# Optimization experiments

Measured on AMD Instinct MI355X. Metric: run time of the kernel, lower is better.

Reference implementation:

```python
import jax, jax.numpy as jnp
import numpy as np

B, L, DM, DI, N, K, NL, DTR, VOCAB, P = 8, 256, 1024, 2048, 16, 4, 4, 128, 99, 97


def setup_inputs() -> dict:
    key = jax.random.key(0)
    ks = jax.random.split(key, 12)
    tokens = jax.random.randint(ks[0], (B, L), 0, VOCAB)
    tok_emb = 0.02 * jax.random.normal(ks[1], (VOCAB, DM), dtype=jnp.float32)
    pos_emb = 0.02 * jax.random.normal(ks[2], (L, DM), dtype=jnp.float32)
    ln_w = jnp.ones((NL, DM), jnp.float32)
    ln_b = jnp.zeros((NL, DM), jnp.float32)
    in_proj_w = jax.random.normal(ks[3], (NL, 2 * DI, DM), dtype=jnp.float32) / np.sqrt(DM)
    conv_w = jax.random.normal(ks[4], (NL, DI, K), dtype=jnp.float32) / np.sqrt(K)
    conv_b = jnp.zeros((NL, DI), jnp.float32)
    xproj_w = jax.random.normal(ks[5], (NL, DTR + 2 * N, DI), dtype=jnp.float32) / np.sqrt(DI)
    s = DTR ** -0.5
    dt_w = jax.random.uniform(ks[6], (NL, DI, DTR), minval=-s, maxval=s, dtype=jnp.float32)
    dt = jnp.exp(jax.random.uniform(ks[7], (NL, DI), dtype=jnp.float32) * (np.log(0.1) - np.log(0.001)) + np.log(0.001))
    dt = jnp.clip(dt, 1e-4)
    dt_b = dt + jnp.log(-jnp.expm1(-dt))
    A_log = jnp.broadcast_to(jnp.log(jnp.arange(1, N + 1, dtype=jnp.float32)), (NL, DI, N)) + jnp.zeros((NL, DI, N))
    D_param = jnp.ones((NL, DI), jnp.float32)
    out_proj_w = jax.random.normal(ks[8], (NL, DM, DI), dtype=jnp.float32) / np.sqrt(DI)
    fnorm_w = jnp.ones((DM,), jnp.float32)
    fnorm_b = jnp.zeros((DM,), jnp.float32)
    head_w = jax.random.normal(ks[9], (P, DM), dtype=jnp.float32) / np.sqrt(DM)
    return dict(tokens=tokens, tok_emb=tok_emb, pos_emb=pos_emb, ln_w=ln_w, ln_b=ln_b,
                in_proj_w=in_proj_w, conv_w=conv_w, conv_b=conv_b, xproj_w=xproj_w,
                dt_w=dt_w, dt_b=dt_b, A_log=A_log, D_param=D_param,
                out_proj_w=out_proj_w, fnorm_w=fnorm_w, fnorm_b=fnorm_b, head_w=head_w)


def layernorm(x, w, b):
    m = x.mean(-1, keepdims=True)
    v = ((x - m) ** 2).mean(-1, keepdims=True)
    return (x - m) * jax.lax.rsqrt(v + 1e-5) * w + b


def causal_dw_conv(x, w, b):
    # x: (B,L,DI), w: (DI,K) depthwise, torch Conv1d(padding=K-1)[..., :L] == causal
    Lx = x.shape[1]
    xp = jnp.pad(x, ((0, 0), (K - 1, 0), (0, 0)))
    y = sum(w[:, k] * xp[:, k:k + Lx, :] for k in range(K))
    return y + b


def selective_ssm(x, xpw, dtw, dtb, Alog, Dp):
    # x: (B,L,DI)
    xp = x @ xpw.T                                # (B,L,DTR+2N)
    dt_r = xp[..., :DTR]
    Bm = xp[..., DTR:DTR + N]                     # (B,L,N)
    Cm = xp[..., DTR + N:]                        # (B,L,N)
    delta = jax.nn.softplus(dt_r @ dtw.T + dtb)   # (B,L,DI)
    A = -jnp.exp(Alog)                            # (DI,N)
    dA = jnp.exp(delta[..., None] * A)            # (B,L,DI,N)
    dBx = delta[..., None] * Bm[:, :, None, :] * x[..., None]  # (B,L,DI,N)

    def step(h, inp):
        dA_t, dBx_t, C_t = inp
        h = dA_t * h + dBx_t
        return h, jnp.einsum('bdn,bn->bd', h, C_t)

    h0 = jnp.zeros((x.shape[0], DI, N), x.dtype)
    _, ys = jax.lax.scan(step, h0, (jnp.moveaxis(dA, 1, 0), jnp.moveaxis(dBx, 1, 0), jnp.moveaxis(Cm, 1, 0)))
    y = jnp.moveaxis(ys, 0, 1)                    # (B,L,DI)
    return y + x * Dp


def mamba_block(h, lnw, lnb, ipw, cw, cb, xpw, dtw, dtb, Alog, Dp, opw):
    residual = h
    x = layernorm(h, lnw, lnb)
    xz = x @ ipw.T                                # (B,L,2*DI)
    x_branch, z_gate = xz[..., :DI], xz[..., DI:]
    x_branch = jax.nn.silu(causal_dw_conv(x_branch, cw, cb))
    y = selective_ssm(x_branch, xpw, dtw, dtb, Alog, Dp)
    y = y * jax.nn.silu(z_gate)
    return y @ opw.T + residual


def reference(tokens, tok_emb, pos_emb, ln_w, ln_b, in_proj_w, conv_w, conv_b, xproj_w,
              dt_w, dt_b, A_log, D_param, out_proj_w, fnorm_w, fnorm_b, head_w):
    h = tok_emb[tokens] + pos_emb[None, :tokens.shape[1]]
    for i in range(NL):
        h = mamba_block(h, ln_w[i], ln_b[i], in_proj_w[i], conv_w[i], conv_b[i],
                        xproj_w[i], dt_w[i], dt_b[i], A_log[i], D_param[i], out_proj_w[i])
    h = layernorm(h, fnorm_w, fnorm_b)
    return h[:, -1, :] @ head_w.T                 # (B,P)
```

## Files before the change

### kernel.cpp

```cpp
#include <hip/hip_runtime.h>
#include <hip/hip_bf16.h>
#include <cstdint>
#include <cstddef>

#define B_    8
#define L_    256
#define DM_   1024
#define DI_   2048
#define N_    16
#define K_    4
#define NL_   4
#define DTR_  128
#define P_    97
#define XPD_  160
#define CHUNK_ 32
#define NC_   8

typedef __attribute__((ext_vector_type(8))) short short8;
typedef __attribute__((ext_vector_type(4))) float floatx4;

__device__ __forceinline__ void async16(const void* g, void* l)
{
    __builtin_amdgcn_global_load_lds(
        (const __attribute__((address_space(1))) void*)g,
        (__attribute__((address_space(3))) void*)l,
        16, 0, 0);
}

__device__ __forceinline__ float bf2f(__hip_bfloat16 h) { return __bfloat162float(h); }

__device__ __forceinline__ void cvt8(const float* s, __hip_bfloat16* d)
{
    float4 a = *(const float4*)s;
    float4 b = *(const float4*)(s + 4);
    union { __hip_bfloat16 h[8]; short8 u; } t;
    t.h[0] = __float2bfloat16(a.x); t.h[1] = __float2bfloat16(a.y);
    t.h[2] = __float2bfloat16(a.z); t.h[3] = __float2bfloat16(a.w);
    t.h[4] = __float2bfloat16(b.x); t.h[5] = __float2bfloat16(b.y);
    t.h[6] = __float2bfloat16(b.z); t.h[7] = __float2bfloat16(b.w);
    *(short8*)d = t.u;
}

__global__ __launch_bounds__(256)
void wconv_embed_k(const float* __restrict__ ipw, const float* __restrict__ opw,
                   const float* __restrict__ dtw, const float* __restrict__ xpw,
                   __hip_bfloat16* __restrict__ ipb, __hip_bfloat16* __restrict__ opb,
                   __hip_bfloat16* __restrict__ dtb, __hip_bfloat16* __restrict__ xpb,
                   const int* __restrict__ tokens, const float* __restrict__ te,
                   const float* __restrict__ pe, const float* __restrict__ lw,
                   const float* __restrict__ lb, float* __restrict__ h,
                   __hip_bfloat16* __restrict__ xout)
{
    __shared__ float red[8];
    int blk = blockIdx.x;
    int tid = threadIdx.x;
    if (blk < 13824) {
        if (blk < 8192) {
            size_t i = (size_t)blk * 2048 + tid * 8;
            cvt8(ipw + i, ipb + i);
        } else if (blk < 12288) {
            size_t i = (size_t)(blk - 8192) * 2048 + tid * 8;
            cvt8(opw + i, opb + i);
        } else if (blk < 12800) {
            size_t i = (size_t)(blk - 12288) * 2048 + tid * 8;
            cvt8(dtw + i, dtb + i);
        } else {
            size_t i = (size_t)(blk - 12800) * 2048 + tid * 8;
            int col   = (int)(i & 2047);
            int row   = (int)((i >> 11) & 255);
            int layer = (int)(i >> 19);
            if (row < XPD_) {
                cvt8(xpw + ((size_t)layer * XPD_ + row) * 2048 + col, xpb + i);
            } else {
                union { __hip_bfloat16 h[8]; short8 u; } t;
                #pragma unroll
                for (int j = 0; j < 8; ++j) t.h[j] = __float2bfloat16(0.f);
                *(short8*)(xpb + i) = t.u;
            }
        }
        return;
    }
    int bl = blk - 13824;
    int l  = bl & (L_ - 1);
    int tok = tokens[bl];
    float4 a = *(const float4*)(te + (size_t)tok * DM_ + tid * 4);
    float4 p = *(const float4*)(pe + (size_t)l * DM_ + tid * 4);
    float4 x = make_float4(a.x + p.x, a.y + p.y, a.z + p.z, a.w + p.w);
    size_t base = (size_t)bl * DM_ + tid * 4;
    *(float4*)(h + base) = x;

    float s  = x.x + x.y + x.z + x.w;
    float s2 = x.x * x.x + x.y * x.y + x.z * x.z + x.w * x.w;
    #pragma unroll
    for (int o = 32; o > 0; o >>= 1) {
        s  += __shfl_down(s, o);
        s2 += __shfl_down(s2, o);
    }
    if ((tid & 63) == 0) { red[tid >> 6] = s; red[4 + (tid >> 6)] = s2; }
    __syncthreads();
    float st  = red[0] + red[1] + red[2] + red[3];
    float s2t = red[4] + red[5] + red[6] + red[7];
    float m   = st * (1.f / DM_);
    float var = s2t * (1.f / DM_) - m * m;
    float rs  = rsqrtf(var + 1e-5f);
    float4 wv = *(const float4*)(lw + tid * 4);
    float4 bv = *(const float4*)(lb + tid * 4);
    union { __hip_bfloat16 h[4]; ushort4 u; } t;
    t.h[0] = __float2bfloat16((x.x - m) * rs * wv.x + bv.x);
    t.h[1] = __float2bfloat16((x.y - m) * rs * wv.y + bv.y);
    t.h[2] = __float2bfloat16((x.z - m) * rs * wv.z + bv.z);
    t.h[3] = __float2bfloat16((x.w - m) * rs * wv.w + bv.w);
    *(ushort4*)(xout + base) = t.u;
}

template<int MODE, int TN>
__global__ __launch_bounds__(256)
void gemm_bf16(const __hip_bfloat16* __restrict__ A, int lda,
               const __hip_bfloat16* __restrict__ Bw, int ldb,
               void* __restrict__ Cv, int ldc, int Kp, int Nb,
               const float* __restrict__ bias)
{
    constexpr int JW = (TN == 128) ? 4 : 2;
    __shared__ __hip_bfloat16 As[128 * 32];
    __shared__ __hip_bfloat16 Bs[TN * 32];
    const int tid  = threadIdx.x;
    const int lane = tid & 63;
    const int wid  = tid >> 6;
    const int wm   = wid >> 1, wn = wid & 1;
    const int mbase = blockIdx.y * 128;
    const int nbase = blockIdx.x * TN;
    const int koff  = (MODE == 2 || MODE == 3) ? blockIdx.z * Kp : 0;

    floatx4 acc[4][JW] = {};

    const int f0 = tid * 16;
    const int r0 = f0 >> 6, c0 = f0 & 63;
    const int f1 = f0 + 4096;
    const int r1 = f1 >> 6, c1 = f1 & 63;

    const int fr = lane & 15;
    const int kq = (lane >> 4) * 8;

    for (int k0 = koff; k0 < koff + Kp; k0 += 32) {
        const char* Ag = (const char*)(A + (size_t)mbase * lda + k0);
        const char* Bg = (const char*)(Bw + (size_t)nbase * ldb + k0);
        async16(Ag + (size_t)r0 * lda * 2 + c0, (char*)As + f0);
        async16(Ag + (size_t)r1 * lda * 2 + c1, (char*)As + f1);
        async16(Bg + (size_t)r0 * ldb * 2 + c0, (char*)Bs + f0);
        if constexpr (TN == 128)
            async16(Bg + (size_t)r1 * ldb * 2 + c1, (char*)Bs + f1);
        __syncthreads();

        short8 af[4], bf[JW];
        #pragma unroll
        for (int i = 0; i < 4; ++i) {
            int m = wm * 64 + i * 16 + fr;
            af[i] = *(const short8*)(As + m * 32 + kq);
        }
        #pragma unroll
        for (int j = 0; j < JW; ++j) {
            int n = wn * (TN / 2) + j * 16 + fr;
            bf[j] = *(const short8*)(Bs + n * 32 + kq);
        }
        #pragma unroll
        for (int i = 0; i < 4; ++i)
            #pragma unroll
            for (int j = 0; j < JW; ++j)
                acc[i][j] = __builtin_amdgcn_mfma_f32_16x16x32_bf16(
                    af[i], bf[j], acc[i][j], 0, 0, 0);
        __syncthreads();
    }

    const int cq = lane >> 4;
    float* Cf = (float*)Cv;
    __hip_bfloat16* Ch = (__hip_bfloat16*)Cv;
    size_t zoff = (MODE == 2 || MODE == 3)
                ? (size_t)blockIdx.z * (gridDim.y * 128) * ldc : 0;
    #pragma unroll
    for (int i = 0; i < 4; ++i) {
        #pragma unroll
        for (int j = 0; j < JW; ++j) {
            int col = nbase + wn * (TN / 2) + j * 16 + fr;
            if (MODE == 3 && col >= Nb) continue;
            float bv = (MODE == 5) ? bias[col] : 0.f;
            #pragma unroll
            for (int r = 0; r < 4; ++r) {
                int row = mbase + wm * 64 + i * 16 + cq * 4 + r;
                float v = acc[i][j][r];
                size_t off = zoff + (size_t)row * ldc + col;
                if (MODE == 2 || MODE == 3) {
                    Cf[off] = v;
                } else if (MODE == 5) {
                    v += bv;
                    v = (v > 20.f) ? v : log1pf(__expf(v));
                    Ch[off] = __float2bfloat16(v);
                } else {
                    Ch[off] = __float2bfloat16(v);
                }
            }
        }
    }
}

template<int PARTS>
__global__ __launch_bounds__(256)
void reduce_xp_k(const float* __restrict__ p, float* __restrict__ dst,
                 __hip_bfloat16* __restrict__ dst_b, size_t stride)
{
    size_t i = ((size_t)blockIdx.x * 256 + threadIdx.x) * 4;
    float4 s = *(const float4*)(p + i);
    #pragma unroll
    for (int z = 1; z < PARTS; ++z) {
        float4 v = *(const float4*)(p + z * stride + i);
        s.x += v.x; s.y += v.y; s.z += v.z; s.w += v.w;
    }
    *(float4*)(dst + i) = s;
    union { __hip_bfloat16 h[4]; ushort4 u; } t;
    t.h[0] = __float2bfloat16(s.x);
    t.h[1] = __float2bfloat16(s.y);
    t.h[2] = __float2bfloat16(s.z);
    t.h[3] = __float2bfloat16(s.w);
    *(ushort4*)(dst_b + i) = t.u;
}

template<int PARTS>
__global__ __launch_bounds__(256)
void reduce_ln_k(const float* __restrict__ p, float* __restrict__ h,
                 const float* __restrict__ w, const float* __restrict__ b,
                 __hip_bfloat16* __restrict__ out, size_t stride)
{
    __shared__ float red[8];
    int tid = threadIdx.x;
    size_t base = (size_t)blockIdx.x * DM_ + tid * 4;
    float4 x = *(const float4*)(h + base);
    #pragma unroll
    for (int z = 0; z < PARTS; ++z) {
        float4 v = *(const float4*)(p + z * stride + base);
        x.x += v.x; x.y += v.y; x.z += v.z; x.w += v.w;
    }
    *(float4*)(h + base) = x;

    float s  = x.x + x.y + x.z + x.w;
    float s2 = x.x * x.x + x.y * x.y + x.z * x.z + x.w * x.w;
    #pragma unroll
    for (int o = 32; o > 0; o >>= 1) {
        s  += __shfl_down(s, o);
        s2 += __shfl_down(s2, o);
    }
    if ((tid & 63) == 0) { red[tid >> 6] = s; red[4 + (tid >> 6)] = s2; }
    __syncthreads();
    float st  = red[0] + red[1] + red[2] + red[3];
    float s2t = red[4] + red[5] + red[6] + red[7];
    float m   = st * (1.f / DM_);
    float var = s2t * (1.f / DM_) - m * m;
    float rs  = rsqrtf(var + 1e-5f);
    float4 wv = *(const float4*)(w + tid * 4);
    float4 bv = *(const float4*)(b + tid * 4);
    union { __hip_bfloat16 h[4]; ushort4 u; } t;
    t.h[0] = __float2bfloat16((x.x - m) * rs * wv.x + bv.x);
    t.h[1] = __float2bfloat16((x.y - m) * rs * wv.y + bv.y);
    t.h[2] = __float2bfloat16((x.z - m) * rs * wv.z + bv.z);
    t.h[3] = __float2bfloat16((x.w - m) * rs * wv.w + bv.w);
    *(ushort4*)(out + base) = t.u;
}

__global__ __launch_bounds__(256)
void conv_silu(const __hip_bfloat16* __restrict__ xz, const float* __restrict__ cw,
               const float* __restrict__ cb, __hip_bfloat16* __restrict__ xb_b)
{
    int idx = blockIdx.x * 256 + threadIdx.x;
    int d  = (idx & 255) << 3;
    int bl = idx >> 8;
    int l  = bl & (L_ - 1);
    float4 w[8];
    #pragma unroll
    for (int j = 0; j < 8; ++j) w[j] = *(const float4*)(cw + (d + j) * 4);
    float acc[8];
    {
        float4 b0 = *(const float4*)(cb + d);
        float4 b1 = *(const float4*)(cb + d + 4);
        acc[0] = b0.x; acc[1] = b0.y; acc[2] = b0.z; acc[3] = b0.w;
        acc[4] = b1.x; acc[5] = b1.y; acc[6] = b1.z; acc[7] = b1.w;
    }
    #pragma unroll
    for (int k = 0; k < 4; ++k) {
        int lk = l + k - 3;
        if (lk >= 0) {
            union { short8 u; __hip_bfloat16 h[8]; } xu;
            xu.u = *(const short8*)(xz + (size_t)(bl - l + lk) * (2 * DI_) + d);
            #pragma unroll
            for (int j = 0; j < 8; ++j)
                acc[j] += ((const float*)&w[j])[k] * bf2f(xu.h[j]);
        }
    }
    union { __hip_bfloat16 h[8]; short8 u; } t;
    #pragma unroll
    for (int j = 0; j < 8; ++j) {
        float v = acc[j] / (1.f + __expf(-acc[j]));
        t.h[j] = __float2bfloat16(v);
    }
    *(short8*)(xb_b + (size_t)bl * DI_ + d) = t.u;
}

__global__ __launch_bounds__(256)
void ssm_pass1(const __hip_bfloat16* __restrict__ xb_b,
               const __hip_bfloat16* __restrict__ dlt_b,
               const float* __restrict__ xp, const float* __restrict__ Alog,
               float* __restrict__ Pc, float* __restrict__ Sc)
{
    int blk = blockIdx.x;
    int dgrp = blk & 7, c = (blk >> 3) & 7, b = blk >> 6;
    int d = (dgrp << 8) + threadIdx.x;
    __shared__ float Bsh[CHUNK_][N_];
    for (int i = threadIdx.x; i < CHUNK_ * N_; i += 256) {
        int t = i >> 4, n = i & 15;
        Bsh[t][n] = xp[(size_t)(b * L_ + c * CHUNK_ + t) * XPD_ + DTR_ + n];
    }
    __syncthreads();
    float a[N_], hn[N_], Pn[N_];
    #pragma unroll
    for (int n = 0; n < N_; ++n) {
        a[n] = -__expf(Alog[d * N_ + n]);
        hn[n] = 0.f; Pn[n] = 1.f;
    }
    for (int t = 0; t < CHUNK_; ++t) {
        size_t off = (size_t)(b * L_ + c * CHUNK_ + t) * DI_ + d;
        float dt = bf2f(dlt_b[off]);
        float xv = bf2f(xb_b[off]);
        float dx = dt * xv;
        #pragma unroll
        for (int n = 0; n < N_; ++n) {
            float dA = __expf(dt * a[n]);
            hn[n] = dA * hn[n] + dx * Bsh[t][n];
            Pn[n] *= dA;
        }
    }
    #pragma unroll
    for (int n = 0; n < N_; ++n) {
        size_t o = ((size_t)((b * NC_ + c) * N_ + n)) * DI_ + d;
        Pc[o] = Pn[n]; Sc[o] = hn[n];
    }
}

__global__ __launch_bounds__(256)
void ssm_pass2(const __hip_bfloat16* __restrict__ xb_b,
               const __hip_bfloat16* __restrict__ dlt_b,
               const float* __restrict__ xp, const float* __restrict__ Alog,
               const float* __restrict__ Dp, const __hip_bfloat16* __restrict__ xz,
               const float* __restrict__ Pc, const float* __restrict__ Sc,
               __hip_bfloat16* __restrict__ yout)
{
    int blk = blockIdx.x;
    int dgrp = blk & 7, c = (blk >> 3) & 7, b = blk >> 6;
    int d = (dgrp << 8) + threadIdx.x;
    __shared__ float Bsh[CHUNK_][N_], Csh[CHUNK_][N_];
    for (int i = threadIdx.x; i < CHUNK_ * 2 * N_; i += 256) {
        int t = i >> 5, j = i & 31;
        float v = xp[(size_t)(b * L_ + c * CHUNK_ + t) * XPD_ + DTR_ + j];
        if (j < 16) Bsh[t][j] = v; else Csh[t][j - 16] = v;
    }
    __syncthreads();
    float a[N_], hn[N_];
    #pragma unroll
    for (int n = 0; n < N_; ++n) {
        a[n] = -__expf(Alog[d * N_ + n]);
        hn[n] = 0.f;
    }
    for (int cp = 0; cp < c; ++cp) {
        #pragma unroll
        for (int n = 0; n < N_; ++n) {
            size_t o = ((size_t)((b * NC_ + cp) * N_ + n)) * DI_ + d;
            hn[n] = Pc[o] * hn[n] + Sc[o];
        }
    }
    float dpv = Dp[d];
    for (int t = 0; t < CHUNK_; ++t) {
        int l = c * CHUNK_ + t;
        size_t off = (size_t)(b * L_ + l) * DI_ + d;
        float dt = bf2f(dlt_b[off]);
        float xv = bf2f(xb_b[off]);
        float dx = dt * xv;
        float yv = 0.f;
        #pragma unroll
        for (int n = 0; n < N_; ++n) {
            float dA = __expf(dt * a[n]);
            hn[n] = dA * hn[n] + dx * Bsh[t][n];
            yv += hn[n] * Csh[t][n];
        }
        yv += xv * dpv;
        float z = bf2f(xz[(size_t)(b * L_ + l) * (2 * DI_) + DI_ + d]);
        yout[off] = __float2bfloat16(yv * z / (1.f + __expf(-z)));
    }
}

__global__ __launch_bounds__(256)
void head_ln_k(const float* __restrict__ h, const float* __restrict__ parts,
               size_t pstride,
               const float* __restrict__ fw, const float* __restrict__ fb,
               const float* __restrict__ hw, float* __restrict__ out)
{
    __shared__ float red[4][5];
    int b = blockIdx.x / P_;
    int p = blockIdx.x % P_;
    int tid = threadIdx.x;
    size_t rowoff = ((size_t)(b * L_ + L_ - 1)) * DM_ + tid * 4;
    float4 x  = *(const float4*)(h + rowoff);
    float4 p0 = *(const float4*)(parts + rowoff);
    float4 p1 = *(const float4*)(parts + pstride + rowoff);
    x.x += p0.x + p1.x; x.y += p0.y + p1.y;
    x.z += p0.z + p1.z; x.w += p0.w + p1.w;
    float4 w4 = *(const float4*)(fw + tid * 4);
    float4 b4 = *(const float4*)(fb + tid * 4);
    float4 g4 = *(const float4*)(hw + (size_t)p * DM_ + tid * 4);
    float s  = x.x + x.y + x.z + x.w;
    float s2 = x.x * x.x + x.y * x.y + x.z * x.z + x.w * x.w;
    float t1 = x.x * w4.x * g4.x + x.y * w4.y * g4.y + x.z * w4.z * g4.z + x.w * w4.w * g4.w;
    float t2 = w4.x * g4.x + w4.y * g4.y + w4.z * g4.z + w4.w * g4.w;
    float t3 = b4.x * g4.x + b4.y * g4.y + b4.z * g4.z + b4.w * g4.w;
    #pragma unroll
    for (int o = 32; o > 0; o >>= 1) {
        s  += __shfl_down(s, o);
        s2 += __shfl_down(s2, o);
        t1 += __shfl_down(t1, o);
        t2 += __shfl_down(t2, o);
        t3 += __shfl_down(t3, o);
    }
    if ((tid & 63) == 0) {
        int w = tid >> 6;
        red[w][0] = s; red[w][1] = s2; red[w][2] = t1; red[w][3] = t2; red[w][4] = t3;
    }
    __syncthreads();
    if (tid == 0) {
        float st  = red[0][0] + red[1][0] + red[2][0] + red[3][0];
        float s2t = red[0][1] + red[1][1] + red[2][1] + red[3][1];
        float t1t = red[0][2] + red[1][2] + red[2][2] + red[3][2];
        float t2t = red[0][3] + red[1][3] + red[2][3] + red[3][3];
        float t3t = red[0][4] + red[1][4] + red[2][4] + red[3][4];
        float m   = st * (1.f / DM_);
        float var = s2t * (1.f / DM_) - m * m;
        float rs  = rsqrtf(var + 1e-5f);
        out[blockIdx.x] = rs * (t1t - m * t2t) + t3t;
    }
}

extern "C" void kernel_launch(void* const* d_in, const int* in_sizes, int n_in,
                              void* d_out, int out_size, void* d_ws, size_t ws_size,
                              hipStream_t stream)
{
    const int*   tokens     = (const int*)  d_in[0];
    const float* tok_emb    = (const float*)d_in[1];
    const float* pos_emb    = (const float*)d_in[2];
    const float* ln_w       = (const float*)d_in[3];
    const float* ln_b       = (const float*)d_in[4];
    const float* in_proj_w  = (const float*)d_in[5];
    const float* conv_w     = (const float*)d_in[6];
    const float* conv_b     = (const float*)d_in[7];
    const float* xproj_w    = (const float*)d_in[8];
    const float* dt_w       = (const float*)d_in[9];
    const float* dt_b       = (const float*)d_in[10];
    const float* A_log      = (const float*)d_in[11];
    const float* D_param    = (const float*)d_in[12];
    const float* out_proj_w = (const float*)d_in[13];
    const float* fnorm_w    = (const float*)d_in[14];
    const float* fnorm_b    = (const float*)d_in[15];
    const float* head_w     = (const float*)d_in[16];
    float* out = (float*)d_out;
    float* ws  = (float*)d_ws;

    float* h      = ws;
    float* xp     = h    + 2097152;
    float* Pc     = xp   + 327680;
    float* Sc     = Pc   + 2097152;
    float* part_h = Sc   + 2097152;
    __hip_bfloat16* bfb = (__hip_bfloat16*)(part_h + 4194304);
    __hip_bfloat16* xz_b  = bfb;
    __hip_bfloat16* xln_b = xz_b  + 8388608;
    __hip_bfloat16* y_b   = xln_b + 2097152;
    __hip_bfloat16* xb_b  = y_b   + 4194304;
    __hip_bfloat16* dlt_b = xb_b  + 4194304;
    __hip_bfloat16* xp_b  = dlt_b + 4194304;
    __hip_bfloat16* dtw_b = xp_b  + 327680;
    __hip_bfloat16* ipw_b = dtw_b + 1048576;
    __hip_bfloat16* opw_b = ipw_b + 16777216;
    __hip_bfloat16* xpw_b = opw_b + 8388608;
    float* part_xp = Pc;

    wconv_embed_k<<<13824 + B_ * L_, 256, 0, stream>>>(
        in_proj_w, out_proj_w, dt_w, xproj_w, ipw_b, opw_b, dtw_b, xpw_b,
        tokens, tok_emb, pos_emb, ln_w, ln_b, h, xln_b);

    for (int li = 0; li < NL_; ++li) {
        gemm_bf16<0, 64><<<dim3(2 * DI_ / 64, B_ * L_ / 128), 256, 0, stream>>>(
            xln_b, DM_, ipw_b + (size_t)li * 2 * DI_ * DM_, DM_,
            xz_b, 2 * DI_, DM_, 0, nullptr);

        conv_silu<<<B_ * L_ * DI_ / 8 / 256, 256, 0, stream>>>(
            xz_b, conv_w + li * DI_ * K_, conv_b + li * DI_, xb_b);

        gemm_bf16<3, 128><<<dim3(2, B_ * L_ / 128, 8), 256, 0, stream>>>(
            xb_b, DI_, xpw_b + (size_t)li * 256 * 2048, DI_,
            part_xp, XPD_, DI_ / 8, XPD_, nullptr);
        reduce_xp_k<8><<<B_ * L_ * XPD_ / 1024, 256, 0, stream>>>(
            part_xp, xp, xp_b, (size_t)B_ * L_ * XPD_);

        gemm_bf16<5, 64><<<dim3(DI_ / 64, B_ * L_ / 128), 256, 0, stream>>>(
            xp_b, XPD_, dtw_b + (size_t)li * DI_ * DTR_, DTR_,
            dlt_b, DI_, DTR_, 0, dt_b + li * DI_);

        ssm_pass1<<<B_ * NC_ * (DI_ / 256), 256, 0, stream>>>(
            xb_b, dlt_b, xp, A_log + li * DI_ * N_, Pc, Sc);
        ssm_pass2<<<B_ * NC_ * (DI_ / 256), 256, 0, stream>>>(
            xb_b, dlt_b, xp, A_log + li * DI_ * N_, D_param + li * DI_,
            xz_b, Pc, Sc, y_b);

        gemm_bf16<2, 64><<<dim3(DM_ / 64, B_ * L_ / 128, 2), 256, 0, stream>>>(
            y_b, DI_, opw_b + (size_t)li * DM_ * DI_, DI_,
            part_h, DM_, DI_ / 2, 0, nullptr);

        if (li < NL_ - 1) {
            reduce_ln_k<2><<<B_ * L_, 256, 0, stream>>>(
                part_h, h, ln_w + (li + 1) * DM_, ln_b + (li + 1) * DM_,
                xln_b, (size_t)B_ * L_ * DM_);
        }
    }

    head_ln_k<<<B_ * P_, 256, 0, stream>>>(
        h, part_h, (size_t)B_ * L_ * DM_, fnorm_w, fnorm_b, head_w, out);
}
```

Before: 832.0 us.

## Fuse fp32-to-bf16 weight conversion into GEMM tile loads

Removes the upfront weight conversion kernel and has each GEMM read fp32 weights directly, converting them to bf16 while staging into shared memory. This drops a full pass that wrote bf16 copies of all weights, but weight tiles are now loaded synchronously as fp32, which doubles their byte traffic. Since weights are re-read by every M-block, the extra global reads and conversion work are repeated across blocks. The x_proj padding rows are handled by a bounds check.

```diff
diff --git a/kernel.cpp b/kernel.cpp
--- a/kernel.cpp
+++ b/kernel.cpp
@@ -29,60 +29,17 @@
 
 __device__ __forceinline__ float bf2f(__hip_bfloat16 h) { return __bfloat162float(h); }
 
-__device__ __forceinline__ void cvt8(const float* s, __hip_bfloat16* d)
-{
-    float4 a = *(const float4*)s;
-    float4 b = *(const float4*)(s + 4);
-    union { __hip_bfloat16 h[8]; short8 u; } t;
-    t.h[0] = __float2bfloat16(a.x); t.h[1] = __float2bfloat16(a.y);
-    t.h[2] = __float2bfloat16(a.z); t.h[3] = __float2bfloat16(a.w);
-    t.h[4] = __float2bfloat16(b.x); t.h[5] = __float2bfloat16(b.y);
-    t.h[6] = __float2bfloat16(b.z); t.h[7] = __float2bfloat16(b.w);
-    *(short8*)d = t.u;
-}
-
-__global__ __launch_bounds__(256)
-void wconv_embed_k(const float* __restrict__ ipw, const float* __restrict__ opw,
-                   const float* __restrict__ dtw, const float* __restrict__ xpw,
-                   __hip_bfloat16* __restrict__ ipb, __hip_bfloat16* __restrict__ opb,
-                   __hip_bfloat16* __restrict__ dtb, __hip_bfloat16* __restrict__ xpb,
-                   const int* __restrict__ tokens, const float* __restrict__ te,
-                   const float* __restrict__ pe, const float* __restrict__ lw,
-                   const float* __restrict__ lb, float* __restrict__ h,
-                   __hip_bfloat16* __restrict__ xout)
+__global__ __launch_bounds__(256)
+void embed_ln_k(const int* __restrict__ tokens, const float* __restrict__ te,
+                const float* __restrict__ pe, const float* __restrict__ lw,
+                const float* __restrict__ lb, float* __restrict__ h,
+                __hip_bfloat16* __restrict__ xout)
 {
     __shared__ float red[8];
-    int blk = blockIdx.x;
-    int tid = threadIdx.x;
-    if (blk < 13824) {
-        if (blk < 8192) {
-            size_t i = (size_t)blk * 2048 + tid * 8;
-            cvt8(ipw + i, ipb + i);
-        } else if (blk < 12288) {
-            size_t i = (size_t)(blk - 8192) * 2048 + tid * 8;
-            cvt8(opw + i, opb + i);
-        } else if (blk < 12800) {
-            size_t i = (size_t)(blk - 12288) * 2048 + tid * 8;
-            cvt8(dtw + i, dtb + i);
-        } else {
-            size_t i = (size_t)(blk - 12800) * 2048 + tid * 8;
-            int col   = (int)(i & 2047);
-            int row   = (int)((i >> 11) & 255);
-            int layer = (int)(i >> 19);
-            if (row < XPD_) {
-                cvt8(xpw + ((size_t)layer * XPD_ + row) * 2048 + col, xpb + i);
-            } else {
-                union { __hip_bfloat16 h[8]; short8 u; } t;
-                #pragma unroll
-                for (int j = 0; j < 8; ++j) t.h[j] = __float2bfloat16(0.f);
-                *(short8*)(xpb + i) = t.u;
-            }
-        }
-        return;
-    }
-    int bl = blk - 13824;
+    int bl = blockIdx.x;
     int l  = bl & (L_ - 1);
     int tok = tokens[bl];
+    int tid = threadIdx.x;
     float4 a = *(const float4*)(te + (size_t)tok * DM_ + tid * 4);
     float4 p = *(const float4*)(pe + (size_t)l * DM_ + tid * 4);
     float4 x = make_float4(a.x + p.x, a.y + p.y, a.z + p.z, a.w + p.w);
@@ -115,12 +72,13 @@
 
 template<int MODE, int TN>
 __global__ __launch_bounds__(256)
-void gemm_bf16(const __hip_bfloat16* __restrict__ A, int lda,
-               const __hip_bfloat16* __restrict__ Bw, int ldb,
-               void* __restrict__ Cv, int ldc, int Kp, int Nb,
+void gemm_wf32(const __hip_bfloat16* __restrict__ A, int lda,
+               const float* __restrict__ Bw, int ldb,
+               void* __restrict__ Cv, int ldc, int Kp, int NbRows,
                const float* __restrict__ bias)
 {
-    constexpr int JW = (TN == 128) ? 4 : 2;
+    constexpr int JW  = (TN == 128) ? 4 : 2;
+    constexpr int EPT = (TN * 32) / 256;
     __shared__ __hip_bfloat16 As[128 * 32];
     __shared__ __hip_bfloat16 Bs[TN * 32];
     const int tid  = threadIdx.x;
@@ -138,20 +96,48 @@
     const int f1 = f0 + 4096;
     const int r1 = f1 >> 6, c1 = f1 & 63;
 
+    const int bf   = tid * EPT;
+    const int brow = bf >> 5;
+    const int bcol = bf & 31;
+    const bool bok = (MODE != 3) || (nbase + brow) < NbRows;
+    const float* Bbase = Bw + (size_t)(nbase + brow) * ldb + bcol;
+
     const int fr = lane & 15;
     const int kq = (lane >> 4) * 8;
 
     for (int k0 = koff; k0 < koff + Kp; k0 += 32) {
         const char* Ag = (const char*)(A + (size_t)mbase * lda + k0);
-        const char* Bg = (const char*)(Bw + (size_t)nbase * ldb + k0);
         async16(Ag + (size_t)r0 * lda * 2 + c0, (char*)As + f0);
         async16(Ag + (size_t)r1 * lda * 2 + c1, (char*)As + f1);
-        async16(Bg + (size_t)r0 * ldb * 2 + c0, (char*)Bs + f0);
-        if constexpr (TN == 128)
-            async16(Bg + (size_t)r1 * ldb * 2 + c1, (char*)Bs + f1);
+        {
+            float4 v0 = make_float4(0.f, 0.f, 0.f, 0.f), v1 = v0;
+            if (bok) {
+                v0 = *(const float4*)(Bbase + k0);
+                v1 = *(const float4*)(Bbase + k0 + 4);
+            }
+            union { __hip_bfloat16 h[8]; short8 u; } tb;
+            tb.h[0] = __float2bfloat16(v0.x); tb.h[1] = __float2bfloat16(v0.y);
+            tb.h[2] = __float2bfloat16(v0.z); tb.h[3] = __float2bfloat16(v0.w);
+            tb.h[4] = __float2bfloat16(v1.x); tb.h[5] = __float2bfloat16(v1.y);
+            tb.h[6] = __float2bfloat16(v1.z); tb.h[7] = __float2bfloat16(v1.w);
+            *(short8*)(Bs + bf) = tb.u;
+            if constexpr (EPT == 16) {
+                float4 v2 = make_float4(0.f, 0.f, 0.f, 0.f), v3 = v2;
+                if (bok) {
+                    v2 = *(const float4*)(Bbase + k0 + 8);
+                    v3 = *(const float4*)(Bbase + k0 + 12);
+                }
+                union { __hip_bfloat16 h[8]; short8 u; } tc;
+                tc.h[0] = __float2bfloat16(v2.x); tc.h[1] = __float2bfloat16(v2.y);
+                tc.h[2] = __float2bfloat16(v2.z); tc.h[3] = __float2bfloat16(v2.w);
+                tc.h[4] = __float2bfloat16(v3.x); tc.h[5] = __float2bfloat16(v3.y);
+                tc.h[6] = __float2bfloat16(v3.z); tc.h[7] = __float2bfloat16(v3.w);
+                *(short8*)(Bs + bf + 8) = tc.u;
+            }
+        }
         __syncthreads();
 
-        short8 af[4], bf[JW];
+        short8 af[4], bfr[JW];
         #pragma unroll
         for (int i = 0; i < 4; ++i) {
             int m = wm * 64 + i * 16 + fr;
@@ -160,14 +146,14 @@
         #pragma unroll
         for (int j = 0; j < JW; ++j) {
             int n = wn * (TN / 2) + j * 16 + fr;
-            bf[j] = *(const short8*)(Bs + n * 32 + kq);
+            bfr[j] = *(const short8*)(Bs + n * 32 + kq);
         }
         #pragma unroll
         for (int i = 0; i < 4; ++i)
             #pragma unroll
             for (int j = 0; j < JW; ++j)
                 acc[i][j] = __builtin_amdgcn_mfma_f32_16x16x32_bf16(
-                    af[i], bf[j], acc[i][j], 0, 0, 0);
+                    af[i], bfr[j], acc[i][j], 0, 0, 0);
         __syncthreads();
     }
 
@@ -181,7 +167,7 @@
         #pragma unroll
         for (int j = 0; j < JW; ++j) {
             int col = nbase + wn * (TN / 2) + j * 16 + fr;
-            if (MODE == 3 && col >= Nb) continue;
+            if (MODE == 3 && col >= NbRows) continue;
             float bv = (MODE == 5) ? bias[col] : 0.f;
             #pragma unroll
             for (int r = 0; r < 4; ++r) {
@@ -479,32 +465,27 @@
     __hip_bfloat16* xb_b  = y_b   + 4194304;
     __hip_bfloat16* dlt_b = xb_b  + 4194304;
     __hip_bfloat16* xp_b  = dlt_b + 4194304;
-    __hip_bfloat16* dtw_b = xp_b  + 327680;
-    __hip_bfloat16* ipw_b = dtw_b + 1048576;
-    __hip_bfloat16* opw_b = ipw_b + 16777216;
-    __hip_bfloat16* xpw_b = opw_b + 8388608;
     float* part_xp = Pc;
 
-    wconv_embed_k<<<13824 + B_ * L_, 256, 0, stream>>>(
-        in_proj_w, out_proj_w, dt_w, xproj_w, ipw_b, opw_b, dtw_b, xpw_b,
-        tokens, tok_emb, pos_emb, ln_w, ln_b, h, xln_b);
+    embed_ln_k<<<B_ * L_, 256, 0, stream>>>(tokens, tok_emb, pos_emb,
+                                            ln_w, ln_b, h, xln_b);
 
     for (int li = 0; li < NL_; ++li) {
-        gemm_bf16<0, 64><<<dim3(2 * DI_ / 64, B_ * L_ / 128), 256, 0, stream>>>(
-            xln_b, DM_, ipw_b + (size_t)li * 2 * DI_ * DM_, DM_,
+        gemm_wf32<0, 64><<<dim3(2 * DI_ / 64, B_ * L_ / 128), 256, 0, stream>>>(
+            xln_b, DM_, in_proj_w + (size_t)li * 2 * DI_ * DM_, DM_,
             xz_b, 2 * DI_, DM_, 0, nullptr);
 
         conv_silu<<<B_ * L_ * DI_ / 8 / 256, 256, 0, stream>>>(
             xz_b, conv_w + li * DI_ * K_, conv_b + li * DI_, xb_b);
 
-        gemm_bf16<3, 128><<<dim3(2, B_ * L_ / 128, 8), 256, 0, stream>>>(
-            xb_b, DI_, xpw_b + (size_t)li * 256 * 2048, DI_,
+        gemm_wf32<3, 128><<<dim3(2, B_ * L_ / 128, 8), 256, 0, stream>>>(
+            xb_b, DI_, xproj_w + (size_t)li * XPD_ * DI_, DI_,
             part_xp, XPD_, DI_ / 8, XPD_, nullptr);
         reduce_xp_k<8><<<B_ * L_ * XPD_ / 1024, 256, 0, stream>>>(
             part_xp, xp, xp_b, (size_t)B_ * L_ * XPD_);
 
-        gemm_bf16<5, 64><<<dim3(DI_ / 64, B_ * L_ / 128), 256, 0, stream>>>(
-            xp_b, XPD_, dtw_b + (size_t)li * DI_ * DTR_, DTR_,
+        gemm_wf32<5, 64><<<dim3(DI_ / 64, B_ * L_ / 128), 256, 0, stream>>>(
+            xp_b, XPD_, dt_w + (size_t)li * DI_ * DTR_, DTR_,
             dlt_b, DI_, DTR_, 0, dt_b + li * DI_);
 
         ssm_pass1<<<B_ * NC_ * (DI_ / 256), 256, 0, stream>>>(
@@ -513,8 +494,8 @@
             xb_b, dlt_b, xp, A_log + li * DI_ * N_, D_param + li * DI_,
             xz_b, Pc, Sc, y_b);
 
-        gemm_bf16<2, 64><<<dim3(DM_ / 64, B_ * L_ / 128, 2), 256, 0, stream>>>(
-            y_b, DI_, opw_b + (size_t)li * DM_ * DI_, DI_,
+        gemm_wf32<2, 64><<<dim3(DM_ / 64, B_ * L_ / 128, 2), 256, 0, stream>>>(
+            y_b, DI_, out_proj_w + (size_t)li * DM_ * DI_, DI_,
             part_h, DM_, DI_ / 2, 0, nullptr);
 
         if (li < NL_ - 1) {
```

After: 913.3 us. 1.1x slower.
